# Performance work log

Hardware: AMD Instinct MI355X
Metric: run time of the kernel (lower is better)

Reference implementation:

```python
import jax, jax.numpy as jnp
import numpy as np

D = 1024
H = 16
DH = D // H
DFF = 4096
EPS = 1e-5


def new_gelu(u):
    # HF NewGELUActivation: 0.5*u*(1+tanh(sqrt(2/pi)*(u+0.044715*u^3)))
    c = np.sqrt(2.0 / np.pi).astype(np.float32)
    return 0.5 * u * (1.0 + jnp.tanh(c * (u + 0.044715 * u ** 3)))


def layer_norm(u, g, b):
    mu = jnp.mean(u, axis=-1, keepdims=True)
    var = jnp.mean((u - mu) ** 2, axis=-1, keepdims=True)
    return (u - mu) * jax.lax.rsqrt(var + EPS) * g + b


def setup_inputs() -> dict:
    key = jax.random.key(0)
    ks = jax.random.split(key, 12)
    s = 0.02
    inp = {
        "x": jax.random.normal(ks[0], (4, 1024, D), dtype=jnp.float32),
        "Wq": jax.random.normal(ks[1], (D, D), dtype=jnp.float32) * s,
        "bq": jnp.zeros((D,), jnp.float32),
        "Wk": jax.random.normal(ks[2], (D, D), dtype=jnp.float32) * s,
        "bk": jnp.zeros((D,), jnp.float32),
        "Wv": jax.random.normal(ks[3], (D, D), dtype=jnp.float32) * s,
        "bv": jnp.zeros((D,), jnp.float32),
        "Wo": jax.random.normal(ks[4], (D, D), dtype=jnp.float32) * s,
        "bo": jnp.zeros((D,), jnp.float32),
        "g1": jnp.ones((D,), jnp.float32),
        "b1": jnp.zeros((D,), jnp.float32),
        "W1": jax.random.normal(ks[5], (D, DFF), dtype=jnp.float32) * s,
        "bm1": jnp.zeros((DFF,), jnp.float32),
        "W2": jax.random.normal(ks[6], (DFF, D), dtype=jnp.float32) * s,
        "bm2": jnp.zeros((D,), jnp.float32),
        "g2": jnp.ones((D,), jnp.float32),
        "b2": jnp.zeros((D,), jnp.float32),
    }
    return inp


def reference(x, Wq, bq, Wk, bk, Wv, bv, Wo, bo, g1, b1, W1, bm1, W2, bm2, g2, b2):
    B, S, _ = x.shape
    q = (x @ Wq + bq).reshape(B, S, H, DH)
    k = (x @ Wk + bk).reshape(B, S, H, DH)
    v = (x @ Wv + bv).reshape(B, S, H, DH)
    scores = jnp.einsum("bshd,bthd->bhst", q, k) / np.sqrt(DH).astype(np.float32)
    probs = jax.nn.softmax(scores, axis=-1)
    attn = jnp.einsum("bhst,bthd->bshd", probs, v).reshape(B, S, D)
    attn = attn @ Wo + bo
    x1 = layer_norm(x + attn, g1, b1)
    mlp = new_gelu(x1 @ W1 + bm1) @ W2 + bm2
    out = layer_norm(x1 + mlp, g2, b2)
    return out
```

## Files before the change

kernel.cpp:

```cpp
#include <hip/hip_runtime.h>

#define D_    1024
#define HH    16
#define DHEAD 64
#define DFF_  4096
#define NTOK  4096
#define SQLEN 1024

typedef unsigned short ushort_t;
typedef __attribute__((ext_vector_type(8))) short short8;
typedef __attribute__((ext_vector_type(4))) float floatx4;

#define LOG2E 1.44269504f

__device__ __forceinline__ unsigned short f2bf(float f) {
  union { float f; unsigned u; } x; x.f = f;
  unsigned r = x.u + 0x7fffu + ((x.u >> 16) & 1u);
  return (unsigned short)(r >> 16);
}
__device__ __forceinline__ float bf2f(unsigned short u) {
  union { unsigned u; float f; } x; x.u = ((unsigned)u) << 16;
  return x.f;
}
__device__ __forceinline__ unsigned pack2bf_fast(float a, float b) {
  union { float f; unsigned u; } x, y; x.f = a; y.f = b;
  return __builtin_amdgcn_perm(y.u + 0x8000u, x.u + 0x8000u, 0x07060302u);
}
__device__ __forceinline__ float fast_exp2(float x) {
  return __builtin_amdgcn_exp2f(x);
}
__device__ __forceinline__ float fast_gelu(float u) {
  float u2 = u * u;
  float arg = u * (2.30220414f + 0.10294307f * u2);
  float e = __builtin_amdgcn_exp2f(arg);
  float r = __builtin_amdgcn_rcpf(e + 1.0f);
  return u - u * r;
}

__device__ __forceinline__ void async_ld16(const void* g, void* l) {
  __builtin_amdgcn_global_load_lds(
      (const __attribute__((address_space(1))) unsigned int*)g,
      (__attribute__((address_space(3))) unsigned int*)l, 16, 0, 0);
}

__device__ __forceinline__ unsigned lds_off(const void* p) {
  return (unsigned)(unsigned long long)
      (const __attribute__((address_space(3))) char*)p;
}
__device__ __forceinline__ short8 ds_read128(unsigned addr) {
  short8 r;
  asm volatile("ds_read_b128 %0, %1" : "=v"(r) : "v"(addr));
  return r;
}

__global__ __launch_bounds__(256) void prep_kernel(
    const float* __restrict__ x, const float* __restrict__ Wq,
    const float* __restrict__ Wk, const float* __restrict__ Wv,
    const float* __restrict__ Wo, const float* __restrict__ W1,
    const float* __restrict__ W2,
    ushort_t* __restrict__ xb, ushort_t* __restrict__ wqkvt,
    ushort_t* __restrict__ wot, ushort_t* __restrict__ w1t,
    ushort_t* __restrict__ w2t) {
  int bid = blockIdx.x, tid = threadIdx.x;
  if (bid < 4096) {
    int i = bid * 256 + tid;
    float4 v = ((const float4*)x)[i];
    ushort4 o;
    o.x = f2bf(v.x); o.y = f2bf(v.y); o.z = f2bf(v.z); o.w = f2bf(v.w);
    ((ushort4*)xb)[i] = o;
    return;
  }
  __shared__ float tile[32][33];
  const float* W; ushort_t* T; int K, N, n0, k0;
  if (bid < 8192) {
    int id = bid - 4096, z = id >> 10, xy = id & 1023;
    W = (z == 0) ? Wq : (z == 1) ? Wk : (z == 2) ? Wv : Wo;
    T = (z < 3) ? wqkvt + (size_t)z * D_ * D_ : wot;
    K = D_; N = D_;
    n0 = (xy & 31) * 32; k0 = (xy >> 5) * 32;
  } else if (bid < 12288) {
    int id = bid - 8192;
    W = W1; T = w1t; K = D_; N = DFF_;
    n0 = (id & 127) * 32; k0 = (id >> 7) * 32;
  } else {
    int id = bid - 12288;
    W = W2; T = w2t; K = DFF_; N = D_;
    n0 = (id & 31) * 32; k0 = (id >> 5) * 32;
  }
  int tx = tid & 31, ty = tid >> 5;
#pragma unroll
  for (int i = 0; i < 4; i++)
    tile[ty + i * 8][tx] = W[(size_t)(k0 + ty + i * 8) * N + n0 + tx];
  __syncthreads();
#pragma unroll
  for (int i = 0; i < 4; i++)
    T[(size_t)(n0 + ty + i * 8) * K + k0 + tx] = f2bf(tile[tx][ty + i * 8]);
}

template <int MODE>
__global__ __launch_bounds__(512, 2) void gemm256(
    const ushort_t* __restrict__ A, const ushort_t* __restrict__ Bt,
    int M, int N, int K, int Ks, int nb,
    const float* __restrict__ bias0, const float* __restrict__ bias1,
    const float* __restrict__ bias2,
    ushort_t* __restrict__ o0, ushort_t* __restrict__ o1, ushort_t* __restrict__ o2) {
  __shared__ alignas(16) ushort_t sA[2][2][128 * 64];
  __shared__ alignas(16) ushort_t sB[2][2][128 * 64];
  int tid = threadIdx.x;
  int w = tid >> 6, lane = tid & 63, quad = lane >> 4, l16 = lane & 15;
  int wm = w >> 2, wn = w & 3;

  int sp = blockIdx.x / nb;
  int bid = blockIdx.x - sp * nb;
  int gridN = N >> 8;
  int Tn = nb >> 3;
  int lin = (bid & 7) * Tn + (bid >> 3);
  int ng = gridN << 3;
  int gidx = lin / ng;
  int rem = lin - gidx * ng;
  int m0 = ((gidx << 3) + (rem & 7)) << 8;
  int n0 = (rem >> 3) << 8;
  int kbeg = sp * Ks;
  int nkt = Ks >> 6;

  floatx4 acc[8][4];
#pragma unroll
  for (int i = 0; i < 8; i++)
#pragma unroll
    for (int j = 0; j < 4; j++) acc[i][j] = (floatx4){0.f, 0.f, 0.f, 0.f};

  int s8  = tid >> 3;
  int lcx = (tid & 7) ^ (s8 & 7);
  const ushort_t* gA = A + (size_t)(m0 + s8) * K + kbeg + lcx * 8;
  const ushort_t* gB = Bt + (size_t)(n0 + (s8 & 31) + (s8 >> 5) * 64) * K + kbeg + lcx * 8;
  char* sta = (char*)&sA[0][0][0] + w * 1024;
  char* stb = (char*)&sB[0][0][0] + w * 1024;

  unsigned kof0 = (unsigned)((quad ^ (l16 & 7)) << 4);
  unsigned baseA = lds_off(&sA[0][0][0]) + (unsigned)((wm * 64 + l16) * 128);
  unsigned baseB = lds_off(&sB[0][0][0]) + (unsigned)((wn * 32 + l16) * 128);

#define STG_A(db, h, ko) { const ushort_t* _g = gA + (size_t)(h) * 64 * K + (ko); \
    char* _l = sta + (db) * 32768 + (h) * 16384; \
    async_ld16(_g, _l); async_ld16(_g + (size_t)128 * K, _l + 8192); }
#define STG_B(db, h, ko) { const ushort_t* _g = gB + (size_t)(h) * 32 * K + (ko); \
    char* _l = stb + (db) * 32768 + (h) * 16384; \
    async_ld16(_g, _l); async_ld16(_g + (size_t)128 * K, _l + 8192); }
#define LDSA(db, mq, DST) { unsigned _p = baseA + (db) * 32768u + (mq) * 16384u + kof0; \
    _Pragma("unroll") for (int mt = 0; mt < 4; mt++) { \
      DST[mt][0] = ds_read128(_p + (unsigned)(mt * 2048)); \
      DST[mt][1] = ds_read128((_p + (unsigned)(mt * 2048)) ^ 64u); } }
#define LDSB(db, nq, DST) { unsigned _p = baseB + (db) * 32768u + (nq) * 16384u + kof0; \
    _Pragma("unroll") for (int nt = 0; nt < 2; nt++) { \
      DST[nt][0] = ds_read128(_p + (unsigned)(nt * 2048)); \
      DST[nt][1] = ds_read128((_p + (unsigned)(nt * 2048)) ^ 64u); } }
#define MFMAC(mq, nq, A_, B_) { \
    _Pragma("unroll") for (int mt = 0; mt < 4; mt++) \
    _Pragma("unroll") for (int nt = 0; nt < 2; nt++) { \
      floatx4 c = acc[(mq) * 4 + mt][(nq) * 2 + nt]; \
      c = __builtin_amdgcn_mfma_f32_16x16x32_bf16(A_[mt][0], B_[nt][0], c, 0, 0, 0); \
      c = __builtin_amdgcn_mfma_f32_16x16x32_bf16(A_[mt][1], B_[nt][1], c, 0, 0, 0); \
      acc[(mq) * 4 + mt][(nq) * 2 + nt] = c; } }
#define BAR __builtin_amdgcn_s_barrier()
#define LGKC(n) { asm volatile("s_waitcnt lgkmcnt(" #n ")" ::: "memory"); \
                  __builtin_amdgcn_sched_barrier(0); }
#define VMW4 asm volatile("s_waitcnt vmcnt(4)" ::: "memory")
#define VMW2 asm volatile("s_waitcnt vmcnt(2)" ::: "memory")
#define VMW0 asm volatile("s_waitcnt vmcnt(0)" ::: "memory")
#define PRIO1 __builtin_amdgcn_s_setprio(1)
#define PRIO0 __builtin_amdgcn_s_setprio(0)

  short8 a[4][2], b0[2][2], b1[2][2];

  STG_A(0, 0, 0); STG_B(0, 0, 0); STG_B(0, 1, 0); STG_A(0, 1, 0);
  VMW2; BAR;

  for (int kt = 0; kt < nkt - 1; kt++) {
    int db = kt & 1, dn = db ^ 1;
    int ko = (kt + 1) << 6;
    LDSA(db, 0, a); LDSB(db, 0, b0); LDSB(db, 1, b1);
    STG_A(dn, 0, ko); STG_B(dn, 0, ko);
    LGKC(4); PRIO1; MFMAC(0, 0, a, b0); PRIO0;
    LGKC(0); PRIO1; MFMAC(0, 1, a, b1); PRIO0;
    VMW4; BAR;
    LDSA(db, 1, a);
    STG_B(dn, 1, ko); STG_A(dn, 1, ko);
    LGKC(0); PRIO1; MFMAC(1, 1, a, b1); PRIO0;
             PRIO1; MFMAC(1, 0, a, b0); PRIO0;
    VMW2; BAR;
  }
  {
    int db = (nkt - 1) & 1;
    LDSA(db, 0, a); LDSB(db, 0, b0); LDSB(db, 1, b1);
    LGKC(4); PRIO1; MFMAC(0, 0, a, b0); PRIO0;
    LGKC(0); PRIO1; MFMAC(0, 1, a, b1); PRIO0;
    VMW0; BAR;
    LDSA(db, 1, a);
    LGKC(0); PRIO1; MFMAC(1, 1, a, b1); PRIO0;
             PRIO1; MFMAC(1, 0, a, b0); PRIO0;
  }

  if (MODE == 0) {
#pragma unroll
    for (int bj = 0; bj < 4; bj++) {
      int cg = n0 + wn * 64 + (bj >> 1) * 32 + (bj & 1) * 16 + l16;
      int sel = cg >> 10, nn = cg & 1023;
      const float* bpp = (sel == 0) ? bias0 : ((sel == 1) ? bias1 : bias2);
      float bb = bpp[nn];
      int hh = nn >> 6, dd = nn & 63;
#pragma unroll
      for (int ai = 0; ai < 8; ai++) {
        int rg0 = m0 + wm * 128 + (ai >> 2) * 64 + (ai & 3) * 16 + quad * 4;
        int b0_ = rg0 >> 10, s0 = rg0 & 1023;
        if (sel == 2) {
          ushort4 ov;
          ov.x = f2bf(acc[ai][bj][0] + bb);
          ov.y = f2bf(acc[ai][bj][1] + bb);
          ov.z = f2bf(acc[ai][bj][2] + bb);
          ov.w = f2bf(acc[ai][bj][3] + bb);
          *(ushort4*)(o2 + ((size_t)(b0_ * HH + hh) * DHEAD + dd) * SQLEN + s0) = ov;
        } else {
          ushort_t* dst = sel ? o1 : o0;
          float sc = (sel == 0) ? (0.125f * LOG2E) : 1.0f;
#pragma unroll
          for (int r = 0; r < 4; r++)
            dst[((size_t)(b0_ * HH + hh) * SQLEN + s0 + r) * DHEAD + dd] =
                f2bf((acc[ai][bj][r] + bb) * sc);
        }
      }
    }
  } else {
    size_t rowbase = (size_t)(m0 + wm * 128 + quad * 4) * N + (n0 + wn * 64 + l16);
    if (MODE == 3) rowbase += (size_t)sp * M * N;
    float bb[4];
    if (MODE == 2) {
#pragma unroll
      for (int c = 0; c < 4; c++)
        bb[c] = bias0[(n0 + wn * 64 + c * 16 + l16) & (N - 1)];
    }
#pragma unroll
    for (int ai = 0; ai < 8; ai++) {
#pragma unroll
      for (int r = 0; r < 4; r++) {
        ushort_t* pr = o0 + rowbase + (size_t)((ai >> 2) * 64 + (ai & 3) * 16 + r) * N;
        if (MODE == 2) {
          pr[0]  = f2bf(fast_gelu(acc[ai][0][r] + bb[0]));
          pr[16] = f2bf(fast_gelu(acc[ai][1][r] + bb[1]));
          pr[32] = f2bf(fast_gelu(acc[ai][2][r] + bb[2]));
          pr[48] = f2bf(fast_gelu(acc[ai][3][r] + bb[3]));
        } else {
          pr[0]  = f2bf(acc[ai][0][r]);
          pr[16] = f2bf(acc[ai][1][r]);
          pr[32] = f2bf(acc[ai][2][r]);
          pr[48] = f2bf(acc[ai][3][r]);
        }
      }
    }
  }
#undef STG_A
#undef STG_B
#undef LDSA
#undef LDSB
#undef MFMAC
#undef BAR
#undef LGKC
#undef VMW4
#undef VMW2
#undef VMW0
#undef PRIO1
#undef PRIO0
}

__global__ __launch_bounds__(256) void flash_attn_kernel(const ushort_t* __restrict__ q,
                                                         const ushort_t* __restrict__ k,
                                                         const ushort_t* __restrict__ vt,
                                                         ushort_t* __restrict__ ctx) {
  __shared__ alignas(16) ushort_t sQ[2][128 * 32];
  __shared__ alignas(16) ushort_t sK[2][64 * 32];
  __shared__ alignas(16) ushort_t sVt[2][64 * 32];
  __shared__ alignas(16) char sP[4][2][2][16 * 80];
  int tid = threadIdx.x;
  int w = tid >> 6, lane = tid & 63, quad = lane >> 4, l16 = lane & 15;
  int bh = blockIdx.x, qt = blockIdx.y;
  int b_ = bh >> 4, h_ = bh & 15;

  const ushort_t* Qp = q + ((size_t)bh * SQLEN + qt * 128) * DHEAD;
  const ushort_t* Kp = k + (size_t)bh * SQLEN * DHEAD;
  const ushort_t* Vtp = vt + (size_t)bh * DHEAD * SQLEN;

  int srow = lane >> 2, scol8 = (lane & 3) * 8;

#pragma unroll
  for (int h = 0; h < 2; h++)
#pragma unroll
    for (int p = 0; p < 2; p++)
      async_ld16(Qp + (h * 64 + w * 16 + srow) * 64 + p * 32 + scol8,
                 (char*)sQ + p * 8192 + (h * 64 + w * 16) * 64);

  float l_run[2] = {0.f, 0.f};
  floatx4 o_acc[2][4];
#pragma unroll
  for (int g = 0; g < 2; g++)
#pragma unroll
    for (int dt = 0; dt < 4; dt++) o_acc[g][dt] = (floatx4){0.f, 0.f, 0.f, 0.f};

  for (int kt = 0; kt < 16; kt++) {
    __syncthreads();
#pragma unroll
    for (int t = 0; t < 2; t++) {
      int id = w * 2 + t, panel = id & 1, rg = id >> 1;
      int row = rg * 16 + srow, col = panel * 32 + scol8;
      async_ld16(Kp + kt * 64 * 64 + row * 64 + col,
                 (char*)sK + panel * 4096 + rg * 1024);
      async_ld16(Vtp + (size_t)row * SQLEN + kt * 64 + col,
                 (char*)sVt + panel * 4096 + rg * 1024);
    }
    __syncthreads();

    floatx4 st[2][4];
#pragma unroll
    for (int g = 0; g < 2; g++)
#pragma unroll
      for (int nt = 0; nt < 4; nt++) st[g][nt] = (floatx4){0.f, 0.f, 0.f, 0.f};
#pragma unroll
    for (int kc = 0; kc < 2; kc++) {
      short8 aq0 = *(const short8*)(sQ[kc] + (w * 32 + l16) * 32 + quad * 8);
      short8 aq1 = *(const short8*)(sQ[kc] + (w * 32 + 16 + l16) * 32 + quad * 8);
#pragma unroll
      for (int nt = 0; nt < 4; nt++) {
        short8 kf = *(const short8*)(sK[kc] + (nt * 16 + l16) * 32 + quad * 8);
        st[0][nt] = __builtin_amdgcn_mfma_f32_16x16x32_bf16(kf, aq0, st[0][nt], 0, 0, 0);
        st[1][nt] = __builtin_amdgcn_mfma_f32_16x16x32_bf16(kf, aq1, st[1][nt], 0, 0, 0);
      }
    }

#pragma unroll
    for (int g = 0; g < 2; g++) {
#pragma unroll
      for (int nt = 0; nt < 4; nt++) {
        float p0 = fast_exp2(st[g][nt][0]);
        float p1 = fast_exp2(st[g][nt][1]);
        float p2 = fast_exp2(st[g][nt][2]);
        float p3 = fast_exp2(st[g][nt][3]);
        l_run[g] += (p0 + p1) + (p2 + p3);
        uint2 d2;
        d2.x = pack2bf_fast(p0, p1);
        d2.y = pack2bf_fast(p2, p3);
        *(uint2*)(&sP[w][g][nt >> 1][0] + l16 * 80 + (nt & 1) * 32 + quad * 8) = d2;
      }
    }

#pragma unroll
    for (int kc = 0; kc < 2; kc++) {
      short8 pf0 = *(const short8*)(&sP[w][0][kc][0] + l16 * 80 + quad * 16);
      short8 pf1 = *(const short8*)(&sP[w][1][kc][0] + l16 * 80 + quad * 16);
#pragma unroll
      for (int dt = 0; dt < 4; dt++) {
        short8 vf = *(const short8*)(sVt[kc] + (dt * 16 + l16) * 32 + quad * 8);
        o_acc[0][dt] = __builtin_amdgcn_mfma_f32_16x16x32_bf16(vf, pf0, o_acc[0][dt], 0, 0, 0);
        o_acc[1][dt] = __builtin_amdgcn_mfma_f32_16x16x32_bf16(vf, pf1, o_acc[1][dt], 0, 0, 0);
      }
    }
  }

#pragma unroll
  for (int g = 0; g < 2; g++) {
    float l = l_run[g];
    l += __shfl_xor(l, 16);
    l += __shfl_xor(l, 32);
    float inv = 1.f / fmaxf(l, 1e-30f);
    int s_ = qt * 128 + w * 32 + g * 16 + l16;
    ushort_t* cp = ctx + (size_t)(b_ * SQLEN + s_) * D_ + h_ * DHEAD + quad * 4;
#pragma unroll
    for (int dt = 0; dt < 4; dt++) {
      ushort4 ov;
      ov.x = f2bf(o_acc[g][dt][0] * inv);
      ov.y = f2bf(o_acc[g][dt][1] * inv);
      ov.z = f2bf(o_acc[g][dt][2] * inv);
      ov.w = f2bf(o_acc[g][dt][3] * inv);
      *(ushort4*)(cp + dt * 16) = ov;
    }
  }
}

template <int S, int WB>
__global__ __launch_bounds__(256) void ln_red_kernel(
    const ushort_t* __restrict__ parts, const float* __restrict__ bias,
    const float* __restrict__ res, const float* __restrict__ g,
    const float* __restrict__ b, float* __restrict__ outf,
    ushort_t* __restrict__ outb) {
  int row = blockIdx.x, tid = threadIdx.x;
  float4 v = ((const float4*)(res + (size_t)row * D_))[tid];
  float4 bb = ((const float4*)bias)[tid];
  v.x += bb.x; v.y += bb.y; v.z += bb.z; v.w += bb.w;
#pragma unroll
  for (int s = 0; s < S; s++) {
    ushort4 p = ((const ushort4*)(parts + (size_t)s * NTOK * D_ + (size_t)row * D_))[tid];
    v.x += bf2f(p.x); v.y += bf2f(p.y); v.z += bf2f(p.z); v.w += bf2f(p.w);
  }
  float s1 = v.x + v.y + v.z + v.w;
  float s2 = v.x * v.x + v.y * v.y + v.z * v.z + v.w * v.w;
#pragma unroll
  for (int off = 32; off > 0; off >>= 1) {
    s1 += __shfl_down(s1, off);
    s2 += __shfl_down(s2, off);
  }
  __shared__ float red[10];
  int wid = tid >> 6, lane = tid & 63;
  if (lane == 0) { red[wid] = s1; red[4 + wid] = s2; }
  __syncthreads();
  if (tid == 0) {
    float ts = red[0] + red[1] + red[2] + red[3];
    float ts2 = red[4] + red[5] + red[6] + red[7];
    float mu = ts * (1.f / 1024.f);
    float var = ts2 * (1.f / 1024.f) - mu * mu;
    red[8] = mu;
    red[9] = rsqrtf(var + 1e-5f);
  }
  __syncthreads();
  float mu = red[8], rsg = red[9];
  float4 gv = ((const float4*)g)[tid];
  float4 bv = ((const float4*)b)[tid];
  float4 o;
  o.x = (v.x - mu) * rsg * gv.x + bv.x;
  o.y = (v.y - mu) * rsg * gv.y + bv.y;
  o.z = (v.z - mu) * rsg * gv.z + bv.z;
  o.w = (v.w - mu) * rsg * gv.w + bv.w;
  if (outf) ((float4*)(outf + (size_t)row * D_))[tid] = o;
  if (WB) {
    ushort4 ob;
    ob.x = f2bf(o.x); ob.y = f2bf(o.y); ob.z = f2bf(o.z); ob.w = f2bf(o.w);
    ((ushort4*)(outb + (size_t)row * D_))[tid] = ob;
  }
}

extern "C" void kernel_launch(void* const* d_in, const int* in_sizes, int n_in,
                              void* d_out, int out_size, void* d_ws, size_t ws_size,
                              hipStream_t stream) {
  const float* x   = (const float*)d_in[0];
  const float* Wq  = (const float*)d_in[1];
  const float* bq  = (const float*)d_in[2];
  const float* Wk  = (const float*)d_in[3];
  const float* bk  = (const float*)d_in[4];
  const float* Wv  = (const float*)d_in[5];
  const float* bv  = (const float*)d_in[6];
  const float* Wo  = (const float*)d_in[7];
  const float* bo  = (const float*)d_in[8];
  const float* g1  = (const float*)d_in[9];
  const float* b1  = (const float*)d_in[10];
  const float* W1  = (const float*)d_in[11];
  const float* bm1 = (const float*)d_in[12];
  const float* W2  = (const float*)d_in[13];
  const float* bm2 = (const float*)d_in[14];
  const float* g2  = (const float*)d_in[15];
  const float* b2  = (const float*)d_in[16];
  float* out = (float*)d_out;

  char* ws = (char*)d_ws;
  const size_t MB = 1024 * 1024;
  ushort_t* xb    = (ushort_t*)(ws + 0);
  ushort_t* wqkvt = (ushort_t*)(ws + 8 * MB);
  ushort_t* wot   = (ushort_t*)(ws + 14 * MB);
  ushort_t* w1t   = (ushort_t*)(ws + 16 * MB);
  ushort_t* w2t   = (ushort_t*)(ws + 24 * MB);
  ushort_t* qb    = (ushort_t*)(ws + 32 * MB);
  ushort_t* kb    = (ushort_t*)(ws + 40 * MB);
  ushort_t* vtb   = (ushort_t*)(ws + 48 * MB);
  ushort_t* ctx   = (ushort_t*)(ws + 56 * MB);
  float*    x1    = (float*)   (ws + 64 * MB);
  ushort_t* x1b   = (ushort_t*)(ws + 80 * MB);
  ushort_t* hbuf  = (ushort_t*)(ws + 88 * MB);
  ushort_t* pWo   = (ushort_t*)(ws + 88 * MB);
  ushort_t* pMd   = (ushort_t*)(ws + 32 * MB);
  (void)ws_size; (void)in_sizes; (void)n_in; (void)out_size;

  hipLaunchKernelGGL(prep_kernel, dim3(16384), dim3(256), 0, stream,
                     x, Wq, Wk, Wv, Wo, W1, W2, xb, wqkvt, wot, w1t, w2t);

  hipLaunchKernelGGL((gemm256<0>), dim3(192), dim3(512), 0, stream,
                     xb, wqkvt, NTOK, 3072, D_, 1024, 192, bq, bk, bv, qb, kb, vtb);

  hipLaunchKernelGGL(flash_attn_kernel, dim3(4 * HH, SQLEN / 128), dim3(256), 0, stream,
                     qb, kb, vtb, ctx);

  hipLaunchKernelGGL((gemm256<3>), dim3(256), dim3(512), 0, stream,
                     ctx, wot, NTOK, D_, D_, 256, 64,
                     (const float*)nullptr, (const float*)nullptr,
                     (const float*)nullptr, pWo, (ushort_t*)nullptr, (ushort_t*)nullptr);

  hipLaunchKernelGGL((ln_red_kernel<4, 1>), dim3(NTOK), dim3(256), 0, stream,
                     pWo, bo, x, g1, b1, x1, x1b);

  hipLaunchKernelGGL((gemm256<2>), dim3(256), dim3(512), 0, stream,
                     x1b, w1t, NTOK, DFF_, D_, 1024, 256, bm1, (const float*)nullptr,
                     (const float*)nullptr, hbuf, (ushort_t*)nullptr, (ushort_t*)nullptr);

  hipLaunchKernelGGL((gemm256<3>), dim3(256), dim3(512), 0, stream,
                     hbuf, w2t, NTOK, D_, DFF_, 1024, 64,
                     (const float*)nullptr, (const float*)nullptr,
                     (const float*)nullptr, pMd, (ushort_t*)nullptr, (ushort_t*)nullptr);

  hipLaunchKernelGGL((ln_red_kernel<4, 0>), dim3(NTOK), dim3(256), 0, stream,
                     pMd, bm2, x1, g2, b2, out, (ushort_t*)nullptr);
}
```

Baseline: 312.5 us.

## Finer-grained LDS wait pipelining in GEMM and register-prefetched K/V in attention

The GEMM main loop now issues LDS reads per A-subtile and waits on lgkmcnt incrementally, so MFMAs start as soon as each subtile arrives. The global staging order also changes: three loads are issued in the first half and the vmcnt threshold rises accordingly. The flash attention kernel replaces async global-to-LDS copies with a register prefetch of the next K/V tile, issued right after the barrier so it overlaps with compute. It also raises wave priority around the MFMA sections. This trades more VGPRs and extra LDS store instructions for better overlap of load latency with compute.

```diff
diff --git a/kernel.cpp b/kernel.cpp
--- a/kernel.cpp
+++ b/kernel.cpp
@@ -146,25 +146,33 @@
 #define STG_B(db, h, ko) { const ushort_t* _g = gB + (size_t)(h) * 32 * K + (ko); \
     char* _l = stb + (db) * 32768 + (h) * 16384; \
     async_ld16(_g, _l); async_ld16(_g + (size_t)128 * K, _l + 8192); }
-#define LDSA(db, mq, DST) { unsigned _p = baseA + (db) * 32768u + (mq) * 16384u + kof0; \
-    _Pragma("unroll") for (int mt = 0; mt < 4; mt++) { \
-      DST[mt][0] = ds_read128(_p + (unsigned)(mt * 2048)); \
-      DST[mt][1] = ds_read128((_p + (unsigned)(mt * 2048)) ^ 64u); } }
+#define LDSA1(db, mq, mt, DST) { \
+    unsigned _p = baseA + (db) * 32768u + (mq) * 16384u + (unsigned)((mt) * 2048) + kof0; \
+    DST[mt][0] = ds_read128(_p); \
+    DST[mt][1] = ds_read128(_p ^ 64u); }
 #define LDSB(db, nq, DST) { unsigned _p = baseB + (db) * 32768u + (nq) * 16384u + kof0; \
     _Pragma("unroll") for (int nt = 0; nt < 2; nt++) { \
       DST[nt][0] = ds_read128(_p + (unsigned)(nt * 2048)); \
       DST[nt][1] = ds_read128((_p + (unsigned)(nt * 2048)) ^ 64u); } }
-#define MFMAC(mq, nq, A_, B_) { \
+#define MFMA_MT(mt, mq, nq, A_, B_) { \
+    floatx4 c0 = acc[(mq) * 4 + (mt)][(nq) * 2 + 0]; \
+    floatx4 c1 = acc[(mq) * 4 + (mt)][(nq) * 2 + 1]; \
+    c0 = __builtin_amdgcn_mfma_f32_16x16x32_bf16(A_[mt][0], B_[0][0], c0, 0, 0, 0); \
+    c1 = __builtin_amdgcn_mfma_f32_16x16x32_bf16(A_[mt][0], B_[1][0], c1, 0, 0, 0); \
+    c0 = __builtin_amdgcn_mfma_f32_16x16x32_bf16(A_[mt][1], B_[0][1], c0, 0, 0, 0); \
+    c1 = __builtin_amdgcn_mfma_f32_16x16x32_bf16(A_[mt][1], B_[1][1], c1, 0, 0, 0); \
+    acc[(mq) * 4 + (mt)][(nq) * 2 + 0] = c0; \
+    acc[(mq) * 4 + (mt)][(nq) * 2 + 1] = c1; }
+#define MFMA_FULL(mq, nq, A_, B_) { \
+    _Pragma("unroll") for (int kc = 0; kc < 2; kc++) \
     _Pragma("unroll") for (int mt = 0; mt < 4; mt++) \
-    _Pragma("unroll") for (int nt = 0; nt < 2; nt++) { \
-      floatx4 c = acc[(mq) * 4 + mt][(nq) * 2 + nt]; \
-      c = __builtin_amdgcn_mfma_f32_16x16x32_bf16(A_[mt][0], B_[nt][0], c, 0, 0, 0); \
-      c = __builtin_amdgcn_mfma_f32_16x16x32_bf16(A_[mt][1], B_[nt][1], c, 0, 0, 0); \
-      acc[(mq) * 4 + mt][(nq) * 2 + nt] = c; } }
+    _Pragma("unroll") for (int nt = 0; nt < 2; nt++) \
+      acc[(mq) * 4 + mt][(nq) * 2 + nt] = __builtin_amdgcn_mfma_f32_16x16x32_bf16( \
+          A_[mt][kc], B_[nt][kc], acc[(mq) * 4 + mt][(nq) * 2 + nt], 0, 0, 0); }
 #define BAR __builtin_amdgcn_s_barrier()
 #define LGKC(n) { asm volatile("s_waitcnt lgkmcnt(" #n ")" ::: "memory"); \
                   __builtin_amdgcn_sched_barrier(0); }
-#define VMW4 asm volatile("s_waitcnt vmcnt(4)" ::: "memory")
+#define VMW6 asm volatile("s_waitcnt vmcnt(6)" ::: "memory")
 #define VMW2 asm volatile("s_waitcnt vmcnt(2)" ::: "memory")
 #define VMW0 asm volatile("s_waitcnt vmcnt(0)" ::: "memory")
 #define PRIO1 __builtin_amdgcn_s_setprio(1)
@@ -178,26 +186,44 @@
   for (int kt = 0; kt < nkt - 1; kt++) {
     int db = kt & 1, dn = db ^ 1;
     int ko = (kt + 1) << 6;
-    LDSA(db, 0, a); LDSB(db, 0, b0); LDSB(db, 1, b1);
-    STG_A(dn, 0, ko); STG_B(dn, 0, ko);
-    LGKC(4); PRIO1; MFMAC(0, 0, a, b0); PRIO0;
-    LGKC(0); PRIO1; MFMAC(0, 1, a, b1); PRIO0;
-    VMW4; BAR;
-    LDSA(db, 1, a);
-    STG_B(dn, 1, ko); STG_A(dn, 1, ko);
-    LGKC(0); PRIO1; MFMAC(1, 1, a, b1); PRIO0;
-             PRIO1; MFMAC(1, 0, a, b0); PRIO0;
+    LDSA1(db, 0, 0, a); LDSB(db, 0, b0);
+    LDSA1(db, 0, 1, a); LDSA1(db, 0, 2, a); LDSA1(db, 0, 3, a);
+    LDSB(db, 1, b1);
+    STG_A(dn, 0, ko); STG_B(dn, 0, ko); STG_B(dn, 1, ko);
+    LGKC(10); PRIO1; MFMA_MT(0, 0, 0, a, b0);
+    LGKC(8);         MFMA_MT(1, 0, 0, a, b0);
+    LGKC(6);         MFMA_MT(2, 0, 0, a, b0);
+    LGKC(4);         MFMA_MT(3, 0, 0, a, b0);
+    LGKC(0);         MFMA_FULL(0, 1, a, b1); PRIO0;
+    VMW6; BAR;
+    LDSA1(db, 1, 0, a);
+    LDSA1(db, 1, 1, a); LDSA1(db, 1, 2, a); LDSA1(db, 1, 3, a);
+    STG_A(dn, 1, ko);
+    LGKC(6); PRIO1; MFMA_MT(0, 1, 1, a, b1);
+    LGKC(4);        MFMA_MT(1, 1, 1, a, b1);
+    LGKC(2);        MFMA_MT(2, 1, 1, a, b1);
+    LGKC(0);        MFMA_MT(3, 1, 1, a, b1);
+                    MFMA_FULL(1, 0, a, b0); PRIO0;
     VMW2; BAR;
   }
   {
     int db = (nkt - 1) & 1;
-    LDSA(db, 0, a); LDSB(db, 0, b0); LDSB(db, 1, b1);
-    LGKC(4); PRIO1; MFMAC(0, 0, a, b0); PRIO0;
-    LGKC(0); PRIO1; MFMAC(0, 1, a, b1); PRIO0;
+    LDSA1(db, 0, 0, a); LDSB(db, 0, b0);
+    LDSA1(db, 0, 1, a); LDSA1(db, 0, 2, a); LDSA1(db, 0, 3, a);
+    LDSB(db, 1, b1);
+    LGKC(10); PRIO1; MFMA_MT(0, 0, 0, a, b0);
+    LGKC(8);         MFMA_MT(1, 0, 0, a, b0);
+    LGKC(6);         MFMA_MT(2, 0, 0, a, b0);
+    LGKC(4);         MFMA_MT(3, 0, 0, a, b0);
+    LGKC(0);         MFMA_FULL(0, 1, a, b1); PRIO0;
     VMW0; BAR;
-    LDSA(db, 1, a);
-    LGKC(0); PRIO1; MFMAC(1, 1, a, b1); PRIO0;
-             PRIO1; MFMAC(1, 0, a, b0); PRIO0;
+    LDSA1(db, 1, 0, a);
+    LDSA1(db, 1, 1, a); LDSA1(db, 1, 2, a); LDSA1(db, 1, 3, a);
+    LGKC(6); PRIO1; MFMA_MT(0, 1, 1, a, b1);
+    LGKC(4);        MFMA_MT(1, 1, 1, a, b1);
+    LGKC(2);        MFMA_MT(2, 1, 1, a, b1);
+    LGKC(0);        MFMA_MT(3, 1, 1, a, b1);
+                    MFMA_FULL(1, 0, a, b0); PRIO0;
   }
 
   if (MODE == 0) {
@@ -259,12 +285,13 @@
   }
 #undef STG_A
 #undef STG_B
-#undef LDSA
+#undef LDSA1
 #undef LDSB
-#undef MFMAC
+#undef MFMA_MT
+#undef MFMA_FULL
 #undef BAR
 #undef LGKC
-#undef VMW4
+#undef VMW6
 #undef VMW2
 #undef VMW0
 #undef PRIO1
@@ -304,24 +331,47 @@
 #pragma unroll
     for (int dt = 0; dt < 4; dt++) o_acc[g][dt] = (floatx4){0.f, 0.f, 0.f, 0.f};
 
+  short8 kr[2], vr[2];
+  const ushort_t* gK[2]; const ushort_t* gV[2];
+  ushort_t* lK[2]; ushort_t* lV[2];
+#pragma unroll
+  for (int t = 0; t < 2; t++) {
+    int id = w * 2 + t, panel = id & 1, rg = id >> 1;
+    int row = rg * 16 + srow, col = panel * 32 + scol8;
+    gK[t] = Kp + row * 64 + col;
+    gV[t] = Vtp + (size_t)row * SQLEN + col;
+    lK[t] = (ushort_t*)((char*)sK + panel * 4096 + rg * 1024 + lane * 16);
+    lV[t] = (ushort_t*)((char*)sVt + panel * 4096 + rg * 1024 + lane * 16);
+  }
+
+#pragma unroll
+  for (int t = 0; t < 2; t++) {
+    kr[t] = *(const short8*)(gK[t]);
+    vr[t] = *(const short8*)(gV[t]);
+  }
+
   for (int kt = 0; kt < 16; kt++) {
     __syncthreads();
 #pragma unroll
     for (int t = 0; t < 2; t++) {
-      int id = w * 2 + t, panel = id & 1, rg = id >> 1;
-      int row = rg * 16 + srow, col = panel * 32 + scol8;
-      async_ld16(Kp + kt * 64 * 64 + row * 64 + col,
-                 (char*)sK + panel * 4096 + rg * 1024);
-      async_ld16(Vtp + (size_t)row * SQLEN + kt * 64 + col,
-                 (char*)sVt + panel * 4096 + rg * 1024);
+      *(short8*)lK[t] = kr[t];
+      *(short8*)lV[t] = vr[t];
     }
     __syncthreads();
+    if (kt < 15) {
+#pragma unroll
+      for (int t = 0; t < 2; t++) {
+        kr[t] = *(const short8*)(gK[t] + (kt + 1) * 4096);
+        vr[t] = *(const short8*)(gV[t] + (kt + 1) * 64);
+      }
+    }
 
     floatx4 st[2][4];
 #pragma unroll
     for (int g = 0; g < 2; g++)
 #pragma unroll
       for (int nt = 0; nt < 4; nt++) st[g][nt] = (floatx4){0.f, 0.f, 0.f, 0.f};
+    __builtin_amdgcn_s_setprio(1);
 #pragma unroll
     for (int kc = 0; kc < 2; kc++) {
       short8 aq0 = *(const short8*)(sQ[kc] + (w * 32 + l16) * 32 + quad * 8);
@@ -333,6 +383,7 @@
         st[1][nt] = __builtin_amdgcn_mfma_f32_16x16x32_bf16(kf, aq1, st[1][nt], 0, 0, 0);
       }
     }
+    __builtin_amdgcn_s_setprio(0);
 
 #pragma unroll
     for (int g = 0; g < 2; g++) {
@@ -350,6 +401,7 @@
       }
     }
 
+    __builtin_amdgcn_s_setprio(1);
 #pragma unroll
     for (int kc = 0; kc < 2; kc++) {
       short8 pf0 = *(const short8*)(&sP[w][0][kc][0] + l16 * 80 + quad * 16);
@@ -361,6 +413,7 @@
         o_acc[1][dt] = __builtin_amdgcn_mfma_f32_16x16x32_bf16(vf, pf1, o_acc[1][dt], 0, 0, 0);
       }
     }
+    __builtin_amdgcn_s_setprio(0);
   }
 
 #pragma unroll
```

After: 314.7 us. About the same (+0.7%).

## Restructure GEMM k-loop with full-tile prefetch and immediate-offset LDS reads

Applied to the files above, without the earlier changes.

The bf16 GEMM main loop is unrolled by two with a fixed double-buffer assignment. The whole next k-tile is prefetched at the start of each step, with a single vmcnt(0)+barrier per tile instead of two half-tile barrier phases. LDS fragment reads now use compile-time immediate offsets on precomputed base and XOR registers, and the MFMA order has the k-chunk outermost. This is meant to cut barrier and address-arithmetic overhead in the hot loop. The new loop logic is only correct when the per-split tile count is even, and waiting for all loads each tile may expose more memory latency.

```diff
diff --git a/kernel.cpp b/kernel.cpp
--- a/kernel.cpp
+++ b/kernel.cpp
@@ -46,11 +46,6 @@
 __device__ __forceinline__ unsigned lds_off(const void* p) {
   return (unsigned)(unsigned long long)
       (const __attribute__((address_space(3))) char*)p;
-}
-__device__ __forceinline__ short8 ds_read128(unsigned addr) {
-  short8 r;
-  asm volatile("ds_read_b128 %0, %1" : "=v"(r) : "v"(addr));
-  return r;
 }
 
 __global__ __launch_bounds__(256) void prep_kernel(
@@ -104,8 +99,8 @@
     const float* __restrict__ bias0, const float* __restrict__ bias1,
     const float* __restrict__ bias2,
     ushort_t* __restrict__ o0, ushort_t* __restrict__ o1, ushort_t* __restrict__ o2) {
-  __shared__ alignas(16) ushort_t sA[2][2][128 * 64];
-  __shared__ alignas(16) ushort_t sB[2][2][128 * 64];
+  __shared__ alignas(128) ushort_t sA[2][2][128 * 64];
+  __shared__ alignas(128) ushort_t sB[2][2][128 * 64];
   int tid = threadIdx.x;
   int w = tid >> 6, lane = tid & 63, quad = lane >> 4, l16 = lane & 15;
   int wm = w >> 2, wn = w & 3;
@@ -137,8 +132,10 @@
   char* stb = (char*)&sB[0][0][0] + w * 1024;
 
   unsigned kof0 = (unsigned)((quad ^ (l16 & 7)) << 4);
-  unsigned baseA = lds_off(&sA[0][0][0]) + (unsigned)((wm * 64 + l16) * 128);
-  unsigned baseB = lds_off(&sB[0][0][0]) + (unsigned)((wn * 32 + l16) * 128);
+  unsigned vA  = lds_off(&sA[0][0][0]) + (unsigned)((wm * 64 + l16) * 128) + kof0;
+  unsigned vAx = vA ^ 64u;
+  unsigned vB  = lds_off(&sB[0][0][0]) + (unsigned)((wn * 32 + l16) * 128) + kof0;
+  unsigned vBx = vB ^ 64u;
 
 #define STG_A(db, h, ko) { const ushort_t* _g = gA + (size_t)(h) * 64 * K + (ko); \
     char* _l = sta + (db) * 32768 + (h) * 16384; \
@@ -146,58 +143,60 @@
 #define STG_B(db, h, ko) { const ushort_t* _g = gB + (size_t)(h) * 32 * K + (ko); \
     char* _l = stb + (db) * 32768 + (h) * 16384; \
     async_ld16(_g, _l); async_ld16(_g + (size_t)128 * K, _l + 8192); }
-#define LDSA(db, mq, DST) { unsigned _p = baseA + (db) * 32768u + (mq) * 16384u + kof0; \
-    _Pragma("unroll") for (int mt = 0; mt < 4; mt++) { \
-      DST[mt][0] = ds_read128(_p + (unsigned)(mt * 2048)); \
-      DST[mt][1] = ds_read128((_p + (unsigned)(mt * 2048)) ^ 64u); } }
-#define LDSB(db, nq, DST) { unsigned _p = baseB + (db) * 32768u + (nq) * 16384u + kof0; \
-    _Pragma("unroll") for (int nt = 0; nt < 2; nt++) { \
-      DST[nt][0] = ds_read128(_p + (unsigned)(nt * 2048)); \
-      DST[nt][1] = ds_read128((_p + (unsigned)(nt * 2048)) ^ 64u); } }
-#define MFMAC(mq, nq, A_, B_) { \
+#define DSR(d, bs, lit) asm volatile("ds_read_b128 %0, %1 offset:" lit \
+    : "=v"(d) : "v"(bs))
+#define LDSA_G(L0, L1, L2, L3) { \
+    DSR(a[0][0], vA, L0); DSR(a[0][1], vAx, L0); \
+    DSR(a[1][0], vA, L1); DSR(a[1][1], vAx, L1); \
+    DSR(a[2][0], vA, L2); DSR(a[2][1], vAx, L2); \
+    DSR(a[3][0], vA, L3); DSR(a[3][1], vAx, L3); }
+#define LDSB_G(DST, L0, L1) { \
+    DSR(DST[0][0], vB, L0); DSR(DST[0][1], vBx, L0); \
+    DSR(DST[1][0], vB, L1); DSR(DST[1][1], vBx, L1); }
+#define MFMAQ(mq, nq, B_) { \
+    _Pragma("unroll") for (int kc = 0; kc < 2; kc++) \
     _Pragma("unroll") for (int mt = 0; mt < 4; mt++) \
-    _Pragma("unroll") for (int nt = 0; nt < 2; nt++) { \
-      floatx4 c = acc[(mq) * 4 + mt][(nq) * 2 + nt]; \
-      c = __builtin_amdgcn_mfma_f32_16x16x32_bf16(A_[mt][0], B_[nt][0], c, 0, 0, 0); \
-      c = __builtin_amdgcn_mfma_f32_16x16x32_bf16(A_[mt][1], B_[nt][1], c, 0, 0, 0); \
-      acc[(mq) * 4 + mt][(nq) * 2 + nt] = c; } }
+    _Pragma("unroll") for (int nt = 0; nt < 2; nt++) \
+      acc[(mq) * 4 + mt][(nq) * 2 + nt] = __builtin_amdgcn_mfma_f32_16x16x32_bf16( \
+          a[mt][kc], B_[nt][kc], acc[(mq) * 4 + mt][(nq) * 2 + nt], 0, 0, 0); }
 #define BAR __builtin_amdgcn_s_barrier()
-#define LGKC(n) { asm volatile("s_waitcnt lgkmcnt(" #n ")" ::: "memory"); \
-                  __builtin_amdgcn_sched_barrier(0); }
-#define VMW4 asm volatile("s_waitcnt vmcnt(4)" ::: "memory")
-#define VMW2 asm volatile("s_waitcnt vmcnt(2)" ::: "memory")
+#define LGK0 { asm volatile("s_waitcnt lgkmcnt(0)" ::: "memory"); \
+               __builtin_amdgcn_sched_barrier(0); }
 #define VMW0 asm volatile("s_waitcnt vmcnt(0)" ::: "memory")
 #define PRIO1 __builtin_amdgcn_s_setprio(1)
 #define PRIO0 __builtin_amdgcn_s_setprio(0)
+#define GTILE(A00, A01, A02, A03, A10, A11, A12, A13, B00, B01, B10, B11) { \
+    LDSA_G(A00, A01, A02, A03); LDSB_G(b0, B00, B01); LDSB_G(b1, B10, B11); \
+    LGK0; PRIO1; MFMAQ(0, 0, b0); MFMAQ(0, 1, b1); PRIO0; \
+    LDSA_G(A10, A11, A12, A13); \
+    LGK0; PRIO1; MFMAQ(1, 1, b1); MFMAQ(1, 0, b0); PRIO0; }
+#define GTILE0 GTILE("0", "2048", "4096", "6144", \
+                     "16384", "18432", "20480", "22528", \
+                     "0", "2048", "16384", "18432")
+#define GTILE1 GTILE("32768", "34816", "36864", "38912", \
+                     "49152", "51200", "53248", "55296", \
+                     "32768", "34816", "49152", "51200")
 
   short8 a[4][2], b0[2][2], b1[2][2];
 
   STG_A(0, 0, 0); STG_B(0, 0, 0); STG_B(0, 1, 0); STG_A(0, 1, 0);
-  VMW2; BAR;
-
-  for (int kt = 0; kt < nkt - 1; kt++) {
-    int db = kt & 1, dn = db ^ 1;
-    int ko = (kt + 1) << 6;
-    LDSA(db, 0, a); LDSB(db, 0, b0); LDSB(db, 1, b1);
-    STG_A(dn, 0, ko); STG_B(dn, 0, ko);
-    LGKC(4); PRIO1; MFMAC(0, 0, a, b0); PRIO0;
-    LGKC(0); PRIO1; MFMAC(0, 1, a, b1); PRIO0;
-    VMW4; BAR;
-    LDSA(db, 1, a);
-    STG_B(dn, 1, ko); STG_A(dn, 1, ko);
-    LGKC(0); PRIO1; MFMAC(1, 1, a, b1); PRIO0;
-             PRIO1; MFMAC(1, 0, a, b0); PRIO0;
-    VMW2; BAR;
+  VMW0; BAR;
+
+  for (int kt = 0; kt + 2 < nkt; kt += 2) {
+    int ko1 = (kt + 1) << 6, ko2 = (kt + 2) << 6;
+    STG_A(1, 0, ko1); STG_B(1, 0, ko1); STG_B(1, 1, ko1); STG_A(1, 1, ko1);
+    GTILE0;
+    VMW0; BAR;
+    STG_A(0, 0, ko2); STG_B(0, 0, ko2); STG_B(0, 1, ko2); STG_A(0, 1, ko2);
+    GTILE1;
+    VMW0; BAR;
   }
   {
-    int db = (nkt - 1) & 1;
-    LDSA(db, 0, a); LDSB(db, 0, b0); LDSB(db, 1, b1);
-    LGKC(4); PRIO1; MFMAC(0, 0, a, b0); PRIO0;
-    LGKC(0); PRIO1; MFMAC(0, 1, a, b1); PRIO0;
+    int ko1 = (nkt - 1) << 6;
+    STG_A(1, 0, ko1); STG_B(1, 0, ko1); STG_B(1, 1, ko1); STG_A(1, 1, ko1);
+    GTILE0;
     VMW0; BAR;
-    LDSA(db, 1, a);
-    LGKC(0); PRIO1; MFMAC(1, 1, a, b1); PRIO0;
-             PRIO1; MFMAC(1, 0, a, b0); PRIO0;
+    GTILE1;
   }
 
   if (MODE == 0) {
@@ -259,16 +258,18 @@
   }
 #undef STG_A
 #undef STG_B
-#undef LDSA
-#undef LDSB
-#undef MFMAC
+#undef DSR
+#undef LDSA_G
+#undef LDSB_G
+#undef MFMAQ
 #undef BAR
-#undef LGKC
-#undef VMW4
-#undef VMW2
+#undef LGK0
 #undef VMW0
 #undef PRIO1
 #undef PRIO0
+#undef GTILE
+#undef GTILE0
+#undef GTILE1
 }
 
 __global__ __launch_bounds__(256) void flash_attn_kernel(const ushort_t* __restrict__ q,
```

Measured after the change: 319.6 us. +2.3%, slower.

## Double-buffer K/V tiles in flash attention with async prefetch and explicit LDS reads

Applied to the files above, without the earlier changes.

The flash attention kernel now double-buffers the K and V^T tiles in LDS. The next tile is issued via global_load_lds before computing the current one, which removes the two full barriers per iteration that serialized load and compute. Fragment loads are rewritten as inline ds_read_b128 with immediate offsets, followed by explicit lgkmcnt waits and s_setprio around the MFMA blocks. This doubles the K/V LDS footprint and depends on hand-placed waitcnt and barrier ordering for correctness.

```diff
diff --git a/kernel.cpp b/kernel.cpp
--- a/kernel.cpp
+++ b/kernel.cpp
@@ -51,6 +51,10 @@
   short8 r;
   asm volatile("ds_read_b128 %0, %1" : "=v"(r) : "v"(addr));
   return r;
+}
+__device__ __forceinline__ void ds_write64(unsigned addr, unsigned lo, unsigned hi) {
+  unsigned long long v = ((unsigned long long)hi << 32) | lo;
+  asm volatile("ds_write_b64 %0, %1" :: "v"(addr), "v"(v));
 }
 
 __global__ __launch_bounds__(256) void prep_kernel(
@@ -276,8 +280,8 @@
                                                          const ushort_t* __restrict__ vt,
                                                          ushort_t* __restrict__ ctx) {
   __shared__ alignas(16) ushort_t sQ[2][128 * 32];
-  __shared__ alignas(16) ushort_t sK[2][64 * 32];
-  __shared__ alignas(16) ushort_t sVt[2][64 * 32];
+  __shared__ alignas(16) ushort_t sK[2][2][64 * 32];
+  __shared__ alignas(16) ushort_t sVt[2][2][64 * 32];
   __shared__ alignas(16) char sP[4][2][2][16 * 80];
   int tid = threadIdx.x;
   int w = tid >> 6, lane = tid & 63, quad = lane >> 4, l16 = lane & 15;
@@ -297,6 +301,27 @@
       async_ld16(Qp + (h * 64 + w * 16 + srow) * 64 + p * 32 + scol8,
                  (char*)sQ + p * 8192 + (h * 64 + w * 16) * 64);
 
+#define STG_KV(kt_, buf_) { \
+    _Pragma("unroll") for (int t = 0; t < 2; t++) { \
+      int id = w * 2 + t, panel = id & 1, rg = id >> 1; \
+      int row = rg * 16 + srow, col = panel * 32 + scol8; \
+      async_ld16(Kp + (kt_) * 64 * 64 + row * 64 + col, \
+                 (char*)sK + (buf_) * 8192 + panel * 4096 + rg * 1024); \
+      async_ld16(Vtp + (size_t)row * SQLEN + (kt_) * 64 + col, \
+                 (char*)sVt + (buf_) * 8192 + panel * 4096 + rg * 1024); } }
+#define FBAR __builtin_amdgcn_s_barrier()
+#define FLGK0 { asm volatile("s_waitcnt lgkmcnt(0)" ::: "memory"); \
+                __builtin_amdgcn_sched_barrier(0); }
+#define FVMW0 asm volatile("s_waitcnt vmcnt(0)" ::: "memory")
+#define FDSR(d, bs, lit) asm volatile("ds_read_b128 %0, %1 offset:" lit \
+    : "=v"(d) : "v"(bs))
+
+  unsigned bQ  = lds_off(&sQ[0][0]) + (unsigned)(w * 2048 + l16 * 64 + quad * 16);
+  unsigned bK0 = lds_off(&sK[0][0][0]) + (unsigned)(l16 * 64 + quad * 16);
+  unsigned bV0 = lds_off(&sVt[0][0][0]) + (unsigned)(l16 * 64 + quad * 16);
+  unsigned bPw = lds_off(&sP[0][0][0][0]) + (unsigned)(w * 5120 + l16 * 80 + quad * 8);
+  unsigned bPr = lds_off(&sP[0][0][0][0]) + (unsigned)(w * 5120 + l16 * 80 + quad * 16);
+
   float l_run[2] = {0.f, 0.f};
   floatx4 o_acc[2][4];
 #pragma unroll
@@ -304,35 +329,38 @@
 #pragma unroll
     for (int dt = 0; dt < 4; dt++) o_acc[g][dt] = (floatx4){0.f, 0.f, 0.f, 0.f};
 
+  STG_KV(0, 0);
+  FVMW0; FBAR;
+
   for (int kt = 0; kt < 16; kt++) {
-    __syncthreads();
-#pragma unroll
-    for (int t = 0; t < 2; t++) {
-      int id = w * 2 + t, panel = id & 1, rg = id >> 1;
-      int row = rg * 16 + srow, col = panel * 32 + scol8;
-      async_ld16(Kp + kt * 64 * 64 + row * 64 + col,
-                 (char*)sK + panel * 4096 + rg * 1024);
-      async_ld16(Vtp + (size_t)row * SQLEN + kt * 64 + col,
-                 (char*)sVt + panel * 4096 + rg * 1024);
-    }
-    __syncthreads();
-
+    unsigned bo_ = (unsigned)((kt & 1) * 8192);
+    if (kt < 15) STG_KV(kt + 1, (kt & 1) ^ 1);
+
+    short8 qf[2][2], kf[4][2];
+    FDSR(qf[0][0], bQ, "0");    FDSR(qf[1][0], bQ, "1024");
+    FDSR(qf[0][1], bQ, "8192"); FDSR(qf[1][1], bQ, "9216");
+    {
+      unsigned bKc = bK0 + bo_;
+      FDSR(kf[0][0], bKc, "0");    FDSR(kf[0][1], bKc, "4096");
+      FDSR(kf[1][0], bKc, "1024"); FDSR(kf[1][1], bKc, "5120");
+      FDSR(kf[2][0], bKc, "2048"); FDSR(kf[2][1], bKc, "6144");
+      FDSR(kf[3][0], bKc, "3072"); FDSR(kf[3][1], bKc, "7168");
+    }
+    FLGK0;
     floatx4 st[2][4];
 #pragma unroll
     for (int g = 0; g < 2; g++)
 #pragma unroll
       for (int nt = 0; nt < 4; nt++) st[g][nt] = (floatx4){0.f, 0.f, 0.f, 0.f};
-#pragma unroll
-    for (int kc = 0; kc < 2; kc++) {
-      short8 aq0 = *(const short8*)(sQ[kc] + (w * 32 + l16) * 32 + quad * 8);
-      short8 aq1 = *(const short8*)(sQ[kc] + (w * 32 + 16 + l16) * 32 + quad * 8);
+    __builtin_amdgcn_s_setprio(1);
+#pragma unroll
+    for (int kc = 0; kc < 2; kc++)
 #pragma unroll
       for (int nt = 0; nt < 4; nt++) {
-        short8 kf = *(const short8*)(sK[kc] + (nt * 16 + l16) * 32 + quad * 8);
-        st[0][nt] = __builtin_amdgcn_mfma_f32_16x16x32_bf16(kf, aq0, st[0][nt], 0, 0, 0);
-        st[1][nt] = __builtin_amdgcn_mfma_f32_16x16x32_bf16(kf, aq1, st[1][nt], 0, 0, 0);
+        st[0][nt] = __builtin_amdgcn_mfma_f32_16x16x32_bf16(kf[nt][kc], qf[0][kc], st[0][nt], 0, 0, 0);
+        st[1][nt] = __builtin_amdgcn_mfma_f32_16x16x32_bf16(kf[nt][kc], qf[1][kc], st[1][nt], 0, 0, 0);
       }
-    }
+    __builtin_amdgcn_s_setprio(0);
 
 #pragma unroll
     for (int g = 0; g < 2; g++) {
@@ -343,24 +371,34 @@
         float p2 = fast_exp2(st[g][nt][2]);
         float p3 = fast_exp2(st[g][nt][3]);
         l_run[g] += (p0 + p1) + (p2 + p3);
-        uint2 d2;
-        d2.x = pack2bf_fast(p0, p1);
-        d2.y = pack2bf_fast(p2, p3);
-        *(uint2*)(&sP[w][g][nt >> 1][0] + l16 * 80 + (nt & 1) * 32 + quad * 8) = d2;
+        ds_write64(bPw + (unsigned)(g * 2560 + (nt >> 1) * 1280 + (nt & 1) * 32),
+                   pack2bf_fast(p0, p1), pack2bf_fast(p2, p3));
       }
     }
-
-#pragma unroll
-    for (int kc = 0; kc < 2; kc++) {
-      short8 pf0 = *(const short8*)(&sP[w][0][kc][0] + l16 * 80 + quad * 16);
-      short8 pf1 = *(const short8*)(&sP[w][1][kc][0] + l16 * 80 + quad * 16);
+    asm volatile("" ::: "memory");
+
+    short8 pf[2][2], vf[4][2];
+    FDSR(pf[0][0], bPr, "0");    FDSR(pf[0][1], bPr, "1280");
+    FDSR(pf[1][0], bPr, "2560"); FDSR(pf[1][1], bPr, "3840");
+    {
+      unsigned bVc = bV0 + bo_;
+      FDSR(vf[0][0], bVc, "0");    FDSR(vf[0][1], bVc, "4096");
+      FDSR(vf[1][0], bVc, "1024"); FDSR(vf[1][1], bVc, "5120");
+      FDSR(vf[2][0], bVc, "2048"); FDSR(vf[2][1], bVc, "6144");
+      FDSR(vf[3][0], bVc, "3072"); FDSR(vf[3][1], bVc, "7168");
+    }
+    FLGK0;
+    __builtin_amdgcn_s_setprio(1);
+#pragma unroll
+    for (int kc = 0; kc < 2; kc++)
 #pragma unroll
       for (int dt = 0; dt < 4; dt++) {
-        short8 vf = *(const short8*)(sVt[kc] + (dt * 16 + l16) * 32 + quad * 8);
-        o_acc[0][dt] = __builtin_amdgcn_mfma_f32_16x16x32_bf16(vf, pf0, o_acc[0][dt], 0, 0, 0);
-        o_acc[1][dt] = __builtin_amdgcn_mfma_f32_16x16x32_bf16(vf, pf1, o_acc[1][dt], 0, 0, 0);
+        o_acc[0][dt] = __builtin_amdgcn_mfma_f32_16x16x32_bf16(vf[dt][kc], pf[0][kc], o_acc[0][dt], 0, 0, 0);
+        o_acc[1][dt] = __builtin_amdgcn_mfma_f32_16x16x32_bf16(vf[dt][kc], pf[1][kc], o_acc[1][dt], 0, 0, 0);
       }
-    }
+    __builtin_amdgcn_s_setprio(0);
+
+    FVMW0; FBAR;
   }
 
 #pragma unroll
@@ -381,6 +419,11 @@
       *(ushort4*)(cp + dt * 16) = ov;
     }
   }
+#undef STG_KV
+#undef FBAR
+#undef FLGK0
+#undef FVMW0
+#undef FDSR
 }
 
 template <int S, int WB>
```

Measured after the change: 318.4 us. About the same (+1.9%).
